# Performance work log

Hardware: AMD Instinct MI355X
Metric: run time of the kernel (lower is better)

The kernel has to match this reference:

```python
import jax, jax.numpy as jnp
import numpy as np

N_EMBD = 1024
N_HEADS = 16
D_K = N_EMBD // N_HEADS


def setup_inputs() -> dict:
    key = jax.random.key(0)
    k1, k2, k3, k4, k5 = jax.random.split(key, 5)
    B, T, E = 4, 2048, N_EMBD
    scale = 1.0 / np.sqrt(E)
    inputs = jax.random.normal(k1, (B, T, E), dtype=jnp.float32)
    W_qkv = jax.random.normal(k2, (3 * E, E), dtype=jnp.float32) * scale
    b_qkv = jax.random.normal(k3, (3 * E,), dtype=jnp.float32) * 0.01
    W_out = jax.random.normal(k4, (E, E), dtype=jnp.float32) * scale
    b_out = jax.random.normal(k5, (E,), dtype=jnp.float32) * 0.01
    return {"inputs": inputs, "W_qkv": W_qkv, "b_qkv": b_qkv,
            "W_out": W_out, "b_out": b_out}


def reference(inputs, W_qkv, b_qkv, W_out, b_out):
    B, T, E = inputs.shape
    H, dk = N_HEADS, D_K
    # fused QKV projection: [B,T,3E]
    qkv = jnp.einsum('bte,fe->btf', inputs, W_qkv) + b_qkv
    # reshape to [B,T,H,3*dk] then to [B,H,T,3*dk], split into q,k,v
    qkv = qkv.reshape(B, T, H, 3 * dk).transpose(0, 2, 1, 3)
    q, k, v = jnp.split(qkv, 3, axis=-1)  # each [B,H,T,dk]
    scores = jnp.einsum('bhqd,bhkd->bhqk', q, k) / np.sqrt(dk)
    causal = jnp.tril(jnp.ones((T, T), dtype=bool))
    scores = jnp.where(causal, scores, -jnp.inf)
    attn = jax.nn.softmax(scores, axis=-1)
    out = jnp.einsum('bhqk,bhkd->bhqd', attn, v)  # [B,H,T,dk]
    out = out.transpose(0, 2, 1, 3).reshape(B, T, E)
    return jnp.einsum('bte,fe->btf', out, W_out) + b_out
```

## Files before the change

kernel.cpp:

```cpp
#include <hip/hip_runtime.h>
#include <stdint.h>


#define DEVFN static __device__ __forceinline__

typedef __attribute__((ext_vector_type(8))) __bf16 bf16x8;
typedef __attribute__((ext_vector_type(8))) ushort ushort8v;
typedef __attribute__((ext_vector_type(4))) float float4v;

#define AS1 __attribute__((address_space(1)))
#define AS3 __attribute__((address_space(3)))

DEVFN ushort f2bf(float f) {
  __bf16 h = (__bf16)f;
  union { __bf16 h; ushort u; } c; c.h = h;
  return c.u;
}

__global__ void cast3_f32_bf16(const float* __restrict__ a, int na,
                               const float* __restrict__ b, int nb,
                               const float* __restrict__ c, int nc,
                               ushort* __restrict__ out) {
  int total = na + nb + nc;
  int stride = gridDim.x * blockDim.x * 4;
  for (int j = (blockIdx.x * blockDim.x + threadIdx.x) * 4; j + 3 < total; j += stride) {
    const float* src;
    if (j < na) src = a + j;
    else if (j < na + nb) src = b + (j - na);
    else src = c + (j - na - nb);
    float4 v = *reinterpret_cast<const float4*>(src);
    ushort4 o;
    o.x = f2bf(v.x); o.y = f2bf(v.y); o.z = f2bf(v.z); o.w = f2bf(v.w);
    *reinterpret_cast<ushort4*>(out + j) = o;
  }
}

template<bool OUT_BF16, bool QSCALE, bool V_SPLIT>
__global__ __launch_bounds__(256) void gemm_bt(
    const ushort* __restrict__ A, const ushort* __restrict__ B,
    const float* __restrict__ bias, void* __restrict__ Cout,
    ushort* __restrict__ vt,
    int M, int N, int K) {
  __shared__ ushort lds_a[2][128 * 32];
  __shared__ ushort lds_b[2][128 * 32];
  const int tid = threadIdx.x;
  const int lane = tid & 63;
  const int w = tid >> 6;
  const int wr = w >> 1, wc = w & 1;
  const int l15 = lane & 15, lg = lane >> 4;

  const int nwg = (int)(gridDim.x * gridDim.y);
  const int orig = (int)(blockIdx.y * gridDim.x + blockIdx.x);
  const int cpx = nwg >> 3;
  const int swz = ((orig & 7) * cpx) + (orig >> 3);
  const int bx = swz % (int)gridDim.x, by = swz / (int)gridDim.x;
  const int m0 = by * 128, n0 = bx * 128;

  const int srow = tid >> 2;
  const int sch = tid & 3;
  const int schs = sch ^ ((srow >> 1) & 3);
  const ushort* ga0 = A + (size_t)(m0 + srow) * K + schs * 8;
  const ushort* gb0 = B + (size_t)(n0 + srow) * K + schs * 8;
  const ushort* ga1 = A + (size_t)(m0 + srow + 64) * K + schs * 8;
  const ushort* gb1 = B + (size_t)(n0 + srow + 64) * K + schs * 8;

#define STAGE(buf, k0)                                                                             \
  {                                                                                                \
    __builtin_amdgcn_global_load_lds((const AS1 uint32_t*)(ga0 + (k0)), (AS3 uint32_t*)&lds_a[buf][tid * 8], 16, 0, 0);        \
    __builtin_amdgcn_global_load_lds((const AS1 uint32_t*)(gb0 + (k0)), (AS3 uint32_t*)&lds_b[buf][tid * 8], 16, 0, 0);        \
    __builtin_amdgcn_global_load_lds((const AS1 uint32_t*)(ga1 + (k0)), (AS3 uint32_t*)&lds_a[buf][2048 + tid * 8], 16, 0, 0); \
    __builtin_amdgcn_global_load_lds((const AS1 uint32_t*)(gb1 + (k0)), (AS3 uint32_t*)&lds_b[buf][2048 + tid * 8], 16, 0, 0); \
  }

  float4v acc[4][4] = {};

  STAGE(0, 0);
  __syncthreads();

  int cur = 0;
  for (int k0 = 0; k0 < K; k0 += 32) {
    if (k0 + 32 < K) STAGE(cur ^ 1, k0 + 32);

    bf16x8 af[4], bfr[4];
#pragma unroll
    for (int m = 0; m < 4; ++m) {
      int row = wr * 64 + m * 16 + l15;
      af[m] = *reinterpret_cast<const bf16x8*>(&lds_a[cur][row * 32 + ((lg ^ ((row >> 1) & 3)) * 8)]);
    }
#pragma unroll
    for (int n = 0; n < 4; ++n) {
      int row = wc * 64 + n * 16 + l15;
      bfr[n] = *reinterpret_cast<const bf16x8*>(&lds_b[cur][row * 32 + ((lg ^ ((row >> 1) & 3)) * 8)]);
    }
    __builtin_amdgcn_s_setprio(1);
#pragma unroll
    for (int m = 0; m < 4; ++m)
#pragma unroll
      for (int n = 0; n < 4; ++n)
        acc[m][n] = __builtin_amdgcn_mfma_f32_16x16x32_bf16(af[m], bfr[n], acc[m][n], 0, 0, 0);
    __builtin_amdgcn_s_setprio(0);

    __syncthreads();
    cur ^= 1;
  }
#undef STAGE

#pragma unroll
  for (int n = 0; n < 4; ++n) {
    int col = n0 + wc * 64 + n * 16 + l15;
    float bv = bias[col];
    int seg = (col % 192) >> 6;
    float f = (QSCALE && seg == 0) ? 0.125f * 1.44269504f : 1.0f;
    if (V_SPLIT && seg == 2) {
      int h = col / 192;
      int d = (col % 192) - 128;
#pragma unroll
      for (int m = 0; m < 4; ++m) {
#pragma unroll
        for (int r = 0; r < 4; ++r) {
          int rowg = m0 + wr * 64 + m * 16 + lg * 4 + r;
          int bb = rowg >> 11, tt = rowg & 2047;
          vt[((size_t)(bb * 16 + h) * 64 + d) * 2048 + tt] = f2bf(acc[m][n][r] + bv);
        }
      }
    } else {
#pragma unroll
      for (int m = 0; m < 4; ++m) {
#pragma unroll
        for (int r = 0; r < 4; ++r) {
          int rowg = m0 + wr * 64 + m * 16 + lg * 4 + r;
          float vv = (acc[m][n][r] + bv) * f;
          if (OUT_BF16)
            ((ushort*)Cout)[(size_t)rowg * N + col] = f2bf(vv);
          else
            ((float*)Cout)[(size_t)rowg * N + col] = vv;
        }
      }
    }
  }
}

__global__ __launch_bounds__(256) void transpose_v(
    const ushort* __restrict__ qkv, ushort* __restrict__ vt) {
  const int bh = blockIdx.y, b = bh >> 4, h = bh & 15;
  const int w = threadIdx.x >> 6, lane = threadIdx.x & 63;
  const int tc = lane >> 3, dc = lane & 7;
  const int t0 = blockIdx.x * 256 + w * 64 + tc * 8;

  const ushort* src = qkv + (size_t)(b * 2048 + t0) * 3072 + h * 192 + 128 + dc * 8;
  ushort r[8][8];
#pragma unroll
  for (int i = 0; i < 8; ++i) {
    ushort8v v = *reinterpret_cast<const ushort8v*>(src + (size_t)i * 3072);
#pragma unroll
    for (int j = 0; j < 8; ++j) r[i][j] = v[j];
  }
  ushort* dst = vt + ((size_t)bh * 64 + dc * 8) * 2048 + t0;
#pragma unroll
  for (int j = 0; j < 8; ++j) {
    ushort8v o;
#pragma unroll
    for (int i = 0; i < 8; ++i) o[i] = r[i][j];
    *reinterpret_cast<ushort8v*>(dst + (size_t)j * 2048) = o;
  }
}

__global__ __launch_bounds__(512, 6) void attn_kernel(
    const ushort* __restrict__ qkv, const ushort* __restrict__ vt,
    ushort* __restrict__ out) {
  __shared__ ushort k_lds[2][4096];
  __shared__ ushort v_lds[2][4096];
  __shared__ ushort p_lds[8][1024];

  const int qb = (int)gridDim.y - 1 - (int)blockIdx.y;
  const int bh = blockIdx.x;
  const int b = bh >> 4, h = bh & 15;
  const int tid = threadIdx.x, lane = tid & 63, w = tid >> 6;
  const int l15 = lane & 15, lg = lane >> 4;

  const size_t rs = 3072;
  const ushort* qbase = qkv + (size_t)(b * 2048) * rs + h * 192;
  const ushort* kbase = qbase + 64;
  const ushort* vtbase = vt + (size_t)bh * 64 * 2048;

  const int q0 = qb * 128;
  const int q0w = q0 + w * 16;
  const int nt = (qb + 1) * 2;

  bf16x8 qf[2];
#pragma unroll
  for (int kk = 0; kk < 2; ++kk)
    qf[kk] = *reinterpret_cast<const bf16x8*>(
        qbase + (size_t)(q0w + l15) * rs + kk * 32 + lg * 8);

  bf16x8 ones;
#pragma unroll
  for (int e = 0; e < 8; ++e) ones[e] = (__bf16)1.0f;

  const int srow = w * 8 + (lane >> 3);
  const int sch = (lane & 7) ^ ((lane >> 3) & 7);
  const ushort* ksrc = kbase + (size_t)srow * rs + sch * 8;
  const ushort* vsrc = vtbase + (size_t)srow * 2048 + sch * 8;
  const size_t kstep = (size_t)64 * rs;
  const size_t vstep = 64;

  __builtin_amdgcn_global_load_lds((const AS1 uint32_t*)ksrc, (AS3 uint32_t*)&k_lds[0][w * 512 + lane * 8], 16, 0, 0);
  __builtin_amdgcn_global_load_lds((const AS1 uint32_t*)vsrc, (AS3 uint32_t*)&v_lds[0][w * 512 + lane * 8], 16, 0, 0);
  ksrc += kstep; vsrc += vstep;
  __syncthreads();

  float4v oacc[4] = {};
  float4v lacc = {};

  int cur = 0;
  for (int t = 0; t < nt; ++t) {
    if (t + 1 < nt) {
      __builtin_amdgcn_global_load_lds((const AS1 uint32_t*)ksrc, (AS3 uint32_t*)&k_lds[cur ^ 1][w * 512 + lane * 8], 16, 0, 0);
      __builtin_amdgcn_global_load_lds((const AS1 uint32_t*)vsrc, (AS3 uint32_t*)&v_lds[cur ^ 1][w * 512 + lane * 8], 16, 0, 0);
      ksrc += kstep; vsrc += vstep;
    }

    if (t * 64 <= q0w + 15) {
      const ushort* kb = k_lds[cur];
      float4v s[4] = {};
      __builtin_amdgcn_s_setprio(1);
#pragma unroll
      for (int kk = 0; kk < 2; ++kk)
#pragma unroll
        for (int n = 0; n < 4; ++n) {
          int row = n * 16 + l15;
          bf16x8 kf = *reinterpret_cast<const bf16x8*>(&kb[row * 64 + (((kk * 4 + lg) ^ (row & 7)) * 8)]);
          s[n] = __builtin_amdgcn_mfma_f32_16x16x32_bf16(qf[kk], kf, s[n], 0, 0, 0);
        }
      __builtin_amdgcn_s_setprio(0);

      if (t * 64 + 63 > q0w) {
#pragma unroll
        for (int n = 0; n < 4; ++n) {
          int kvg = t * 64 + n * 16 + l15;
#pragma unroll
          for (int r = 0; r < 4; ++r) {
            int qg = q0w + lg * 4 + r;
            if (kvg > qg) s[n][r] = -1e30f;
          }
        }
      }

#pragma unroll
      for (int n = 0; n < 4; ++n) {
#pragma unroll
        for (int r = 0; r < 4; ++r) {
          float p = __builtin_amdgcn_exp2f(s[n][r]);
          int row = lg * 4 + r;
          int col = n * 16 + l15;
          int ch = (col >> 3) ^ (row & 7);
          p_lds[w][row * 64 + ch * 8 + (col & 7)] = f2bf(p);
        }
      }

      bf16x8 pf[2];
#pragma unroll
      for (int kk = 0; kk < 2; ++kk)
        pf[kk] = *reinterpret_cast<const bf16x8*>(&p_lds[w][l15 * 64 + (((kk * 4 + lg) ^ (l15 & 7)) * 8)]);

      const ushort* vb_ = v_lds[cur];
      __builtin_amdgcn_s_setprio(1);
#pragma unroll
      for (int kk = 0; kk < 2; ++kk) {
#pragma unroll
        for (int nd = 0; nd < 4; ++nd) {
          int vr = nd * 16 + l15;
          bf16x8 vf = *reinterpret_cast<const bf16x8*>(&vb_[vr * 64 + (((kk * 4 + lg) ^ (vr & 7)) * 8)]);
          oacc[nd] = __builtin_amdgcn_mfma_f32_16x16x32_bf16(pf[kk], vf, oacc[nd], 0, 0, 0);
        }
        lacc = __builtin_amdgcn_mfma_f32_16x16x32_bf16(pf[kk], ones, lacc, 0, 0, 0);
      }
      __builtin_amdgcn_s_setprio(0);
    }

    __syncthreads();
    cur ^= 1;
  }

  float linv[4];
#pragma unroll
  for (int r = 0; r < 4; ++r) linv[r] = __builtin_amdgcn_rcpf(lacc[r]);
#pragma unroll
  for (int nd = 0; nd < 4; ++nd) {
#pragma unroll
    for (int r = 0; r < 4; ++r) {
      int qg = q0 + w * 16 + lg * 4 + r;
      int col = h * 64 + nd * 16 + l15;
      out[(size_t)(b * 2048 + qg) * 1024 + col] = f2bf(oacc[nd][r] * linv[r]);
    }
  }
}

extern "C" void kernel_launch(void* const* d_in, const int* in_sizes, int n_in,
                              void* d_out, int out_size, void* d_ws, size_t ws_size,
                              hipStream_t stream) {
  (void)in_sizes; (void)n_in; (void)out_size;
  const float* x      = (const float*)d_in[0];
  const float* w_qkv  = (const float*)d_in[1];
  const float* b_qkv  = (const float*)d_in[2];
  const float* w_out  = (const float*)d_in[3];
  const float* b_out  = (const float*)d_in[4];
  float* outp = (float*)d_out;

  const int BT = 4 * 2048;
  const int E = 1024, N3 = 3072;

  char* ws = (char*)d_ws;
  ushort* xb    = (ushort*)ws;  ws += (size_t)BT * E * 2;
  ushort* wqkvb = (ushort*)ws;  ws += (size_t)N3 * E * 2;
  ushort* woutb = (ushort*)ws;  ws += (size_t)E * E * 2;
  ushort* qkvb  = (ushort*)ws;  ws += (size_t)BT * N3 * 2;
  ushort* attb  = (ushort*)ws;  ws += (size_t)BT * E * 2;
  ushort* vtsep = (ushort*)ws;  ws += (size_t)BT * E * 2;
  const size_t needed = (size_t)(ws - (char*)d_ws);
  const bool vsplit = (ws_size >= needed);

  cast3_f32_bf16<<<2048, 256, 0, stream>>>(x, BT * E, w_qkv, N3 * E, w_out, E * E, xb);

  dim3 g1(N3 / 128, BT / 128);
  dim3 gt(8, 64);
  dim3 g2(64, 16);
  dim3 g3(E / 128, BT / 128);

  if (vsplit) {
    gemm_bt<true, true, true><<<g1, 256, 0, stream>>>(xb, wqkvb, b_qkv, qkvb, vtsep, BT, N3, E);
    attn_kernel<<<g2, 512, 0, stream>>>(qkvb, vtsep, attb);
  } else {
    ushort* vtb = xb;
    gemm_bt<true, true, false><<<g1, 256, 0, stream>>>(xb, wqkvb, b_qkv, qkvb, nullptr, BT, N3, E);
    transpose_v<<<gt, 256, 0, stream>>>(qkvb, vtb);
    attn_kernel<<<g2, 512, 0, stream>>>(qkvb, vtb, attb);
  }

  gemm_bt<false, false, false><<<g3, 256, 0, stream>>>(attb, woutb, b_out, outp, nullptr, BT, E, E);
}
```

Baseline: 170.7 us.

## Double attention query tile per block to 256 rows for K/V reuse

```diff
diff --git a/kernel.cpp b/kernel.cpp
--- a/kernel.cpp
+++ b/kernel.cpp
@@ -165,14 +165,15 @@
   }
 }
 
-__global__ __launch_bounds__(512, 6) void attn_kernel(
+__global__ __launch_bounds__(512, 4) void attn_kernel(
     const ushort* __restrict__ qkv, const ushort* __restrict__ vt,
     ushort* __restrict__ out) {
   __shared__ ushort k_lds[2][4096];
   __shared__ ushort v_lds[2][4096];
-  __shared__ ushort p_lds[8][1024];
-
-  const int qb = (int)gridDim.y - 1 - (int)blockIdx.y;
+  __shared__ ushort p_lds[8][2][1024];
+
+  const int y = (int)blockIdx.y;
+  const int qb = (y < 4) ? (7 - y) : (y - 4);
   const int bh = blockIdx.x;
   const int b = bh >> 4, h = bh & 15;
   const int tid = threadIdx.x, lane = tid & 63, w = tid >> 6;
@@ -183,15 +184,17 @@
   const ushort* kbase = qbase + 64;
   const ushort* vtbase = vt + (size_t)bh * 64 * 2048;
 
-  const int q0 = qb * 128;
-  const int q0w = q0 + w * 16;
-  const int nt = (qb + 1) * 2;
-
-  bf16x8 qf[2];
-#pragma unroll
-  for (int kk = 0; kk < 2; ++kk)
-    qf[kk] = *reinterpret_cast<const bf16x8*>(
-        qbase + (size_t)(q0w + l15) * rs + kk * 32 + lg * 8);
+  const int q0 = qb * 256;
+  const int q0w = q0 + w * 32;
+  const int nt = (qb + 1) * 4;
+
+  bf16x8 qf[2][2];
+#pragma unroll
+  for (int hf = 0; hf < 2; ++hf)
+#pragma unroll
+    for (int kk = 0; kk < 2; ++kk)
+      qf[hf][kk] = *reinterpret_cast<const bf16x8*>(
+          qbase + (size_t)(q0w + hf * 16 + l15) * rs + kk * 32 + lg * 8);
 
   bf16x8 ones;
 #pragma unroll
@@ -209,8 +212,8 @@
   ksrc += kstep; vsrc += vstep;
   __syncthreads();
 
-  float4v oacc[4] = {};
-  float4v lacc = {};
+  float4v oacc[2][4] = {};
+  float4v lacc[2] = {};
 
   int cur = 0;
   for (int t = 0; t < nt; ++t) {
@@ -220,78 +223,88 @@
       ksrc += kstep; vsrc += vstep;
     }
 
-    if (t * 64 <= q0w + 15) {
+    if (t * 64 <= q0w + 31) {
       const ushort* kb = k_lds[cur];
-      float4v s[4] = {};
-      __builtin_amdgcn_s_setprio(1);
-#pragma unroll
-      for (int kk = 0; kk < 2; ++kk)
+      const ushort* vb_ = v_lds[cur];
+
+#pragma unroll
+      for (int hf = 0; hf < 2; ++hf) {
+        const int qh = q0w + hf * 16;
+        if (t * 64 > qh + 15) continue;
+
+        float4v s[4] = {};
+        __builtin_amdgcn_s_setprio(1);
+#pragma unroll
+        for (int kk = 0; kk < 2; ++kk)
+#pragma unroll
+          for (int n = 0; n < 4; ++n) {
+            int row = n * 16 + l15;
+            bf16x8 kf = *reinterpret_cast<const bf16x8*>(&kb[row * 64 + (((kk * 4 + lg) ^ (row & 7)) * 8)]);
+            s[n] = __builtin_amdgcn_mfma_f32_16x16x32_bf16(qf[hf][kk], kf, s[n], 0, 0, 0);
+          }
+        __builtin_amdgcn_s_setprio(0);
+
+        if (t * 64 + 63 > qh) {
+#pragma unroll
+          for (int n = 0; n < 4; ++n) {
+            int kvg = t * 64 + n * 16 + l15;
+#pragma unroll
+            for (int r = 0; r < 4; ++r) {
+              int qg = qh + lg * 4 + r;
+              if (kvg > qg) s[n][r] = -1e30f;
+            }
+          }
+        }
+
 #pragma unroll
         for (int n = 0; n < 4; ++n) {
-          int row = n * 16 + l15;
-          bf16x8 kf = *reinterpret_cast<const bf16x8*>(&kb[row * 64 + (((kk * 4 + lg) ^ (row & 7)) * 8)]);
-          s[n] = __builtin_amdgcn_mfma_f32_16x16x32_bf16(qf[kk], kf, s[n], 0, 0, 0);
-        }
-      __builtin_amdgcn_s_setprio(0);
-
-      if (t * 64 + 63 > q0w) {
-#pragma unroll
-        for (int n = 0; n < 4; ++n) {
-          int kvg = t * 64 + n * 16 + l15;
 #pragma unroll
           for (int r = 0; r < 4; ++r) {
-            int qg = q0w + lg * 4 + r;
-            if (kvg > qg) s[n][r] = -1e30f;
+            float p = __builtin_amdgcn_exp2f(s[n][r]);
+            int row = lg * 4 + r;
+            int col = n * 16 + l15;
+            int ch = (col >> 3) ^ (row & 7);
+            p_lds[w][hf][row * 64 + ch * 8 + (col & 7)] = f2bf(p);
           }
         }
+
+        bf16x8 pf[2];
+#pragma unroll
+        for (int kk = 0; kk < 2; ++kk)
+          pf[kk] = *reinterpret_cast<const bf16x8*>(&p_lds[w][hf][l15 * 64 + (((kk * 4 + lg) ^ (l15 & 7)) * 8)]);
+
+        __builtin_amdgcn_s_setprio(1);
+#pragma unroll
+        for (int kk = 0; kk < 2; ++kk) {
+#pragma unroll
+          for (int nd = 0; nd < 4; ++nd) {
+            int vr = nd * 16 + l15;
+            bf16x8 vf = *reinterpret_cast<const bf16x8*>(&vb_[vr * 64 + (((kk * 4 + lg) ^ (vr & 7)) * 8)]);
+            oacc[hf][nd] = __builtin_amdgcn_mfma_f32_16x16x32_bf16(pf[kk], vf, oacc[hf][nd], 0, 0, 0);
+          }
+          lacc[hf] = __builtin_amdgcn_mfma_f32_16x16x32_bf16(pf[kk], ones, lacc[hf], 0, 0, 0);
+        }
+        __builtin_amdgcn_s_setprio(0);
       }
-
-#pragma unroll
-      for (int n = 0; n < 4; ++n) {
-#pragma unroll
-        for (int r = 0; r < 4; ++r) {
-          float p = __builtin_amdgcn_exp2f(s[n][r]);
-          int row = lg * 4 + r;
-          int col = n * 16 + l15;
-          int ch = (col >> 3) ^ (row & 7);
-          p_lds[w][row * 64 + ch * 8 + (col & 7)] = f2bf(p);
-        }
-      }
-
-      bf16x8 pf[2];
-#pragma unroll
-      for (int kk = 0; kk < 2; ++kk)
-        pf[kk] = *reinterpret_cast<const bf16x8*>(&p_lds[w][l15 * 64 + (((kk * 4 + lg) ^ (l15 & 7)) * 8)]);
-
-      const ushort* vb_ = v_lds[cur];
-      __builtin_amdgcn_s_setprio(1);
-#pragma unroll
-      for (int kk = 0; kk < 2; ++kk) {
-#pragma unroll
-        for (int nd = 0; nd < 4; ++nd) {
-          int vr = nd * 16 + l15;
-          bf16x8 vf = *reinterpret_cast<const bf16x8*>(&vb_[vr * 64 + (((kk * 4 + lg) ^ (vr & 7)) * 8)]);
-          oacc[nd] = __builtin_amdgcn_mfma_f32_16x16x32_bf16(pf[kk], vf, oacc[nd], 0, 0, 0);
-        }
-        lacc = __builtin_amdgcn_mfma_f32_16x16x32_bf16(pf[kk], ones, lacc, 0, 0, 0);
-      }
-      __builtin_amdgcn_s_setprio(0);
     }
 
     __syncthreads();
     cur ^= 1;
   }
 
-  float linv[4];
-#pragma unroll
-  for (int r = 0; r < 4; ++r) linv[r] = __builtin_amdgcn_rcpf(lacc[r]);
-#pragma unroll
-  for (int nd = 0; nd < 4; ++nd) {
-#pragma unroll
-    for (int r = 0; r < 4; ++r) {
-      int qg = q0 + w * 16 + lg * 4 + r;
-      int col = h * 64 + nd * 16 + l15;
-      out[(size_t)(b * 2048 + qg) * 1024 + col] = f2bf(oacc[nd][r] * linv[r]);
+#pragma unroll
+  for (int hf = 0; hf < 2; ++hf) {
+    float linv[4];
+#pragma unroll
+    for (int r = 0; r < 4; ++r) linv[r] = __builtin_amdgcn_rcpf(lacc[hf][r]);
+#pragma unroll
+    for (int nd = 0; nd < 4; ++nd) {
+#pragma unroll
+      for (int r = 0; r < 4; ++r) {
+        int qg = q0w + hf * 16 + lg * 4 + r;
+        int col = h * 64 + nd * 16 + l15;
+        out[(size_t)(b * 2048 + qg) * 1024 + col] = f2bf(oacc[hf][nd][r] * linv[r]);
+      }
     }
   }
 }
@@ -324,7 +337,7 @@
 
   dim3 g1(N3 / 128, BT / 128);
   dim3 gt(8, 64);
-  dim3 g2(64, 16);
+  dim3 g2(64, 8);
   dim3 g3(E / 128, BT / 128);
 
   if (vsplit) {
```

Result: slower. 182.2 us (+6.8%).
